# Kernel optimization log

Hardware: AMD Instinct MI355X
Metric: run time of the kernel (lower is better)

## Reference

```python
import jax, jax.numpy as jnp
import numpy as np

D_HIDN = 768
N_HEAD = 12
D_HEAD = 64
LN_EPS = 1e-5


def setup_inputs() -> dict:
    key = jax.random.key(0)
    ks = jax.random.split(key, 16)
    B, S, D = 4, 2048, D_HIDN
    s = 0.02
    inputs = jax.random.normal(ks[0], (B, S, D), dtype=jnp.float32)
    attn_mask = jax.random.uniform(ks[1], (B, S, S)) < 0.1
    Wq = jax.random.normal(ks[2], (D, D), jnp.float32) * s
    bq = jnp.zeros((D,), jnp.float32)
    Wk = jax.random.normal(ks[3], (D, D), jnp.float32) * s
    bk = jnp.zeros((D,), jnp.float32)
    Wv = jax.random.normal(ks[4], (D, D), jnp.float32) * s
    bv = jnp.zeros((D,), jnp.float32)
    g1 = jnp.ones((D,), jnp.float32)
    beta1 = jnp.zeros((D,), jnp.float32)
    W1 = jax.random.normal(ks[5], (D, 4 * D), jnp.float32) * s
    b1 = jnp.zeros((4 * D,), jnp.float32)
    W2 = jax.random.normal(ks[6], (4 * D, D), jnp.float32) * s
    b2 = jnp.zeros((D,), jnp.float32)
    g2 = jnp.ones((D,), jnp.float32)
    beta2 = jnp.zeros((D,), jnp.float32)
    return dict(inputs=inputs, attn_mask=attn_mask, Wq=Wq, bq=bq, Wk=Wk, bk=bk,
                Wv=Wv, bv=bv, g1=g1, beta1=beta1, W1=W1, b1=b1, W2=W2, b2=b2,
                g2=g2, beta2=beta2)


def _layernorm(x, g, b):
    mu = jnp.mean(x, axis=-1, keepdims=True)
    var = jnp.mean(jnp.square(x - mu), axis=-1, keepdims=True)
    return (x - mu) * jax.lax.rsqrt(var + LN_EPS) * g + b


def reference(inputs, attn_mask, Wq, bq, Wk, bk, Wv, bv, g1, beta1,
              W1, b1, W2, b2, g2, beta2):
    B, S, D = inputs.shape
    H, Dh = N_HEAD, D_HEAD
    # QKV projections -> [B, H, S, Dh]
    q = (inputs @ Wq + bq).reshape(B, S, H, Dh).transpose(0, 2, 1, 3)
    k = (inputs @ Wk + bk).reshape(B, S, H, Dh).transpose(0, 2, 1, 3)
    v = (inputs @ Wv + bv).reshape(B, S, H, Dh).transpose(0, 2, 1, 3)
    scale = 1.0 / (Dh ** 0.5)
    scores = jnp.einsum('bhqd,bhkd->bhqk', q, k) * scale  # [B,H,S,S]
    scores = jnp.where(attn_mask[:, None, :, :], jnp.float32(-1e9), scores)
    attn = jax.nn.softmax(scores, axis=-1)
    ctx = jnp.einsum('bhqk,bhkd->bhqd', attn, v)  # [B,H,S,Dh]
    attn_out = ctx.transpose(0, 2, 1, 3).reshape(B, S, D)
    # Add & Norm 1
    ffn_in = _layernorm(attn_out + inputs, g1, beta1)
    # FFN (note: no activation in the original module)
    ffn_out = (ffn_in @ W1 + b1) @ W2 + b2
    # Add & Norm 2
    return _layernorm(ffn_out + ffn_in, g2, beta2)
```

## Files before the change

kernel.cpp:

```cpp
#include <hip/hip_runtime.h>

typedef unsigned short u16;
typedef __attribute__((ext_vector_type(8))) __bf16 bf16x8;
typedef __attribute__((ext_vector_type(4))) __bf16 bf16x4;
typedef __attribute__((ext_vector_type(4))) float f32x4;

#define DEV __device__ __forceinline__

DEV u16 f2bf(float f) {
  unsigned u = __builtin_bit_cast(unsigned, f);
  u += 0x7FFFu + ((u >> 16) & 1u);
  return (u16)(u >> 16);
}
DEV float bf2f(u16 u) {
  unsigned v = (unsigned)u << 16;
  return __builtin_bit_cast(float, v);
}

DEV void stage16(const void* g, void* l) {
  __builtin_amdgcn_global_load_lds((const __attribute__((address_space(1))) void*)g,
                                   (__attribute__((address_space(3))) void*)l, 16, 0, 0);
}

DEV f32x4 mfma32(bf16x8 a, bf16x8 b, f32x4 c) {
  return __builtin_amdgcn_mfma_f32_16x16x32_bf16(a, b, c, 0, 0, 0);
}

DEV void transpose_tile(const float* __restrict__ src, u16* __restrict__ dst,
                        int R, int C, int bx, int by, int t, float (*tile)[33]) {
  int tx = t & 31, ty = t >> 5;
  int c0 = bx * 32, r0 = by * 32;
#pragma unroll
  for (int i = 0; i < 4; ++i)
    tile[ty + i * 8][tx] = src[(size_t)(r0 + ty + i * 8) * C + c0 + tx];
  __syncthreads();
#pragma unroll
  for (int i = 0; i < 4; ++i)
    dst[(size_t)(c0 + ty + i * 8) * R + r0 + tx] = f2bf(tile[tx][ty + i * 8]);
}

__global__ __launch_bounds__(256) void prep_all(
    const float* __restrict__ Wq, const float* __restrict__ Wk, const float* __restrict__ Wv,
    const float* __restrict__ W1, const float* __restrict__ W2,
    const float* __restrict__ inputs, const int* __restrict__ maskI,
    u16* __restrict__ WqkvT, u16* __restrict__ W1b, u16* __restrict__ W2T,
    u16* __restrict__ Xb, unsigned long long* __restrict__ bits) {
  __shared__ float tile[32][33];
  const int t = threadIdx.x;
  const int bid = blockIdx.x;
  if (bid < 1728) {
    int z = bid / 576, rem = bid % 576;
    const float* src = (z == 0) ? Wq : (z == 1 ? Wk : Wv);
    transpose_tile(src, WqkvT + (size_t)z * 768 * 768, 768, 768, rem % 24, rem / 24, t, tile);
  } else if (bid < 4032) {
    int rem = bid - 1728;
    transpose_tile(W2, W2T, 3072, 768, rem % 24, rem / 24, t, tile);
  } else if (bid < 6336) {
    int i = (bid - 4032) * 256 + t;
    float4 f = ((const float4*)W1)[i];
    ushort4 u;
    u.x = f2bf(f.x); u.y = f2bf(f.y); u.z = f2bf(f.z); u.w = f2bf(f.w);
    ((ushort4*)W1b)[i] = u;
  } else if (bid < 12480) {
    int i = (bid - 6336) * 256 + t;
    float4 f = ((const float4*)inputs)[i];
    ushort4 u;
    u.x = f2bf(f.x); u.y = f2bf(f.y); u.z = f2bf(f.z); u.w = f2bf(f.w);
    ((ushort4*)Xb)[i] = u;
  } else {
    int lb = bid - 12480;
    int lane = t & 63;
    int w0 = (lb * 4 + (t >> 6)) * 4;
#pragma unroll
    for (int j = 0; j < 4; ++j) {
      int v = maskI[(size_t)(w0 + j) * 64 + lane];
      unsigned long long bm = __ballot(v != 0);
      if (lane == 0) bits[w0 + j] = bm;
    }
  }
}

template <int MODE>
DEV void gemm_body(u16 (*Als)[128 * 32], u16 (*Bls)[128 * 32],
                   const u16* __restrict__ A, const u16* __restrict__ Bt, int K,
                   const float* __restrict__ b0, const float* __restrict__ b1p,
                   const float* __restrict__ b2p, const u16* __restrict__ resid,
                   u16* __restrict__ outQ, u16* __restrict__ outK, u16* __restrict__ outV,
                   u16* __restrict__ outB, int bx, int by, int bz) {
  const int t = threadIdx.x;
  const int lane = t & 63, wv = t >> 6;
  const int wm = wv & 1, wn = wv >> 1;
  const int lrow = lane & 15, g = lane >> 4;
  const int m0 = by * 128, n0 = bx * 128;

  int koff = 0, klen = K;
  if (MODE == 2) {
    klen = K >> 1;
    koff = bz * klen;
  }

  f32x4 acc[4][4] = {};

  const int idx0 = t, idx1 = 256 + t;
  const int row0 = idx0 >> 2, sl0 = (idx0 & 3) ^ ((row0 >> 1) & 3);
  const int row1 = idx1 >> 2, sl1 = (idx1 & 3) ^ ((row1 >> 1) & 3);

  auto stage = [&](int k0, int buf) {
    stage16(A + (size_t)(m0 + row0) * K + koff + k0 + sl0 * 8, (char*)Als[buf] + idx0 * 16);
    stage16(Bt + (size_t)(n0 + row0) * K + koff + k0 + sl0 * 8, (char*)Bls[buf] + idx0 * 16);
    stage16(A + (size_t)(m0 + row1) * K + koff + k0 + sl1 * 8, (char*)Als[buf] + idx1 * 16);
    stage16(Bt + (size_t)(n0 + row1) * K + koff + k0 + sl1 * 8, (char*)Bls[buf] + idx1 * 16);
  };

  stage(0, 0);
  __syncthreads();

  int nk = klen >> 5;
  for (int it = 0; it < nk; ++it) {
    int cur = it & 1;
    if (it + 1 < nk) stage((it + 1) << 5, cur ^ 1);
    bf16x8 af[4], bfr[4];
#pragma unroll
    for (int mi = 0; mi < 4; ++mi) {
      int r = wm * 64 + mi * 16 + lrow;
      int sl = g ^ ((r >> 1) & 3);
      af[mi] = *(const bf16x8*)((const char*)Als[cur] + r * 64 + sl * 16);
    }
#pragma unroll
    for (int ni = 0; ni < 4; ++ni) {
      int r = wn * 64 + ni * 16 + lrow;
      int sl = g ^ ((r >> 1) & 3);
      bfr[ni] = *(const bf16x8*)((const char*)Bls[cur] + r * 64 + sl * 16);
    }
    __builtin_amdgcn_s_setprio(1);
#pragma unroll
    for (int mi = 0; mi < 4; ++mi)
#pragma unroll
      for (int ni = 0; ni < 4; ++ni)
        acc[mi][ni] = mfma32(af[mi], bfr[ni], acc[mi][ni]);
    __builtin_amdgcn_s_setprio(0);
    __syncthreads();
  }

#pragma unroll
  for (int mi = 0; mi < 4; ++mi)
#pragma unroll
    for (int ni = 0; ni < 4; ++ni)
#pragma unroll
      for (int reg = 0; reg < 4; ++reg) {
        int gm = m0 + wm * 64 + mi * 16 + g * 4 + reg;
        int gn = n0 + wn * 64 + ni * 16 + lrow;
        float v = acc[mi][ni][reg];
        if (MODE == 0) {
          int p = gn / 768, nn = gn - p * 768;
          const float* bb = (p == 0) ? b0 : (p == 1 ? b1p : b2p);
          v += bb[nn];
          int b = gm >> 11, s = gm & 2047;
          int h = nn >> 6, dh = nn & 63;
          size_t hh = (size_t)(b * 12 + h);
          if (p == 0)      outQ[(hh * 2048 + s) * 64 + dh] = f2bf(v * 0.1803368801f);
          else if (p == 1) outK[(hh * 2048 + s) * 64 + dh] = f2bf(v);
          else             outV[(hh * 64 + dh) * 2048 + s] = f2bf(v);
        } else if (MODE == 2) {
          if (bz == 1) {
            v += b0[gn] + bf2f(resid[(size_t)gm * 768 + gn]);
            outK[(size_t)gm * 768 + gn] = f2bf(v);
          } else {
            outQ[(size_t)gm * 768 + gn] = f2bf(v);
          }
        } else {
          outB[(size_t)gn * 768 + gm] = f2bf(v);
        }
      }
}

template <int MODE, int OCC>
__global__ __launch_bounds__(256, OCC) void gemm_k(
    const u16* __restrict__ A, const u16* __restrict__ Bt, int K,
    const float* __restrict__ b0, const u16* __restrict__ resid,
    u16* __restrict__ out0, u16* __restrict__ out1) {
  __shared__ u16 Als[2][128 * 32];
  __shared__ u16 Bls[2][128 * 32];
  gemm_body<MODE>(Als, Bls, A, Bt, K, b0, nullptr, nullptr, resid,
                  out0, out1, nullptr, nullptr, blockIdx.x, blockIdx.y, blockIdx.z);
}

__global__ __launch_bounds__(256, 4) void fused_gemms(
    const u16* __restrict__ Xb, const u16* __restrict__ WqkvT,
    const float* __restrict__ bq, const float* __restrict__ bk, const float* __restrict__ bv,
    u16* __restrict__ Qb, u16* __restrict__ Kb, u16* __restrict__ Vtb,
    const u16* __restrict__ W1b, const u16* __restrict__ W2T, u16* __restrict__ W12T,
    const float* __restrict__ b1, const float* __restrict__ b2, float* __restrict__ biasEff) {
  __shared__ u16 Als[2][128 * 32];
  __shared__ u16 Bls[2][128 * 32];
  const int bid = blockIdx.x;
  if (bid < 1152) {
    gemm_body<0>(Als, Bls, Xb, WqkvT, 768, bq, bk, bv, nullptr,
                 Qb, Kb, Vtb, nullptr, bid % 18, bid / 18, 0);
  } else if (bid < 1188) {
    int lb = bid - 1152;
    gemm_body<3>(Als, Bls, W1b, W2T, 3072, nullptr, nullptr, nullptr, nullptr,
                 nullptr, nullptr, nullptr, W12T, lb % 6, lb / 6, 0);
  } else {
    const int j = bid - 1188, t = threadIdx.x;
    float s = 0.f;
    for (int k = t; k < 3072; k += 256) s += b1[k] * bf2f(W2T[(size_t)j * 3072 + k]);
    for (int d = 1; d < 64; d <<= 1) s += __shfl_xor(s, d, 64);
    __shared__ float red[4];
    if ((t & 63) == 0) red[t >> 6] = s;
    __syncthreads();
    if (t == 0) biasEff[j] = b2[j] + red[0] + red[1] + red[2] + red[3];
  }
}

__global__ __launch_bounds__(512, 6) void attn_fwd(
    const u16* __restrict__ Q, const u16* __restrict__ Kg, const u16* __restrict__ Vt,
    const unsigned long long* __restrict__ mbits, u16* __restrict__ attn_out) {
  __shared__ u16 Kls[2][64 * 64];
  __shared__ u16 Vls[2][64 * 64];
  __shared__ u16 Pls[8][16 * 64];
  const int t = threadIdx.x, lane = t & 63, wv = t >> 6;
  const int lrow = lane & 15, g = lane >> 4;

  const int fid = blockIdx.x;
  const int swz = (fid & 7) * 96 + (fid >> 3);
  const int bh = swz >> 4, q0 = (swz & 15) * 128;
  const int b = bh / 12, h = bh % 12;
  const u16* Qh = Q + (size_t)bh * 2048 * 64;
  const u16* Kh = Kg + (size_t)bh * 2048 * 64;
  const u16* Vh = Vt + (size_t)bh * 64 * 2048;

  const int qr = q0 + wv * 16 + lrow;
  bf16x8 aq[2];
  aq[0] = *(const bf16x8*)(Qh + (size_t)qr * 64 + g * 8);
  aq[1] = *(const bf16x8*)(Qh + (size_t)qr * 64 + 32 + g * 8);

  bf16x8 ones;
#pragma unroll
  for (int j = 0; j < 8; ++j) ones[j] = (__bf16)1.0f;

  f32x4 acc[4] = {};
  f32x4 lacc = {};

  const int row0 = t >> 3, sl0 = (t & 7) ^ (row0 & 7);
  auto stage = [&](int kt, int buf) {
    stage16(Kh + ((size_t)(kt * 64 + row0)) * 64 + sl0 * 8, (char*)Kls[buf] + t * 16);
    stage16(Vh + (size_t)row0 * 2048 + kt * 64 + sl0 * 8, (char*)Vls[buf] + t * 16);
  };

  const unsigned long long* mrow = mbits + ((size_t)b * 2048 + qr) * 32;
  unsigned long long mb = mrow[0];

  stage(0, 0);
  __syncthreads();

#pragma unroll 2
  for (int kt = 0; kt < 32; ++kt) {
    const int cur = kt & 1;
    if (kt + 1 < 32) stage(kt + 1, cur ^ 1);

    f32x4 sc[4];
#pragma unroll
    for (int c = 0; c < 4; ++c) {
      sc[c] = 0.f;
#pragma unroll
      for (int ks = 0; ks < 2; ++ks) {
        int r = c * 16 + lrow;
        int sl = (ks * 4 + g) ^ (r & 7);
        bf16x8 bk = *(const bf16x8*)((const char*)Kls[cur] + r * 128 + sl * 16);
        sc[c] = mfma32(bk, aq[ks], sc[c]);
      }
    }

    unsigned long long mbn = (kt + 1 < 32) ? mrow[kt + 1] : 0;

    unsigned mlo = (unsigned)mb, mhi = (unsigned)(mb >> 32);
#pragma unroll
    for (int c = 0; c < 4; ++c) {
      unsigned bits = ((c & 2) ? mhi : mlo) >> ((c & 1) * 16 + 4 * g);
#pragma unroll
      for (int reg = 0; reg < 4; ++reg)
        sc[c][reg] = ((bits >> reg) & 1) ? 0.f : __builtin_amdgcn_exp2f(sc[c][reg]);
    }
    mb = mbn;

#pragma unroll
    for (int c = 0; c < 4; ++c) {
      bf16x4 pk;
#pragma unroll
      for (int reg = 0; reg < 4; ++reg) pk[reg] = (__bf16)sc[c][reg];
      int slot = 2 * c + (g >> 1);
      int byte = lrow * 128 + ((slot ^ (lrow & 7)) << 4) + (g & 1) * 8;
      *(bf16x4*)((char*)Pls[wv] + byte) = pk;
    }
    asm volatile("s_waitcnt lgkmcnt(0)" ::: "memory");

#pragma unroll
    for (int ks = 0; ks < 2; ++ks) {
      int slp = (ks * 4 + g) ^ (lrow & 7);
      bf16x8 pa = *(const bf16x8*)((const char*)Pls[wv] + lrow * 128 + slp * 16);
      lacc = mfma32(pa, ones, lacc);
#pragma unroll
      for (int c = 0; c < 4; ++c) {
        int r = c * 16 + lrow;
        int sl = (ks * 4 + g) ^ (r & 7);
        bf16x8 vf = *(const bf16x8*)((const char*)Vls[cur] + r * 128 + sl * 16);
        acc[c] = mfma32(pa, vf, acc[c]);
      }
    }
    __syncthreads();
  }

  float rl[4];
#pragma unroll
  for (int reg = 0; reg < 4; ++reg) rl[reg] = 1.0f / lacc[reg];
#pragma unroll
  for (int c = 0; c < 4; ++c)
#pragma unroll
    for (int reg = 0; reg < 4; ++reg) {
      int q = q0 + wv * 16 + 4 * g + reg;
      int col = h * 64 + c * 16 + lrow;
      attn_out[((size_t)b * 2048 + q) * 768 + col] = f2bf(acc[c][reg] * rl[reg]);
    }
}

__global__ __launch_bounds__(192) void ln_fused2(
    const u16* __restrict__ x1b, const u16* __restrict__ x2b,
    const float* __restrict__ gam, const float* __restrict__ bet,
    float* __restrict__ outf, u16* __restrict__ outb) {
  const int row = blockIdx.x, t = threadIdx.x;
  const size_t base = (size_t)row * 768 + t * 4;
  bf16x4 a = *(const bf16x4*)(x1b + base);
  bf16x4 c = *(const bf16x4*)(x2b + base);
  float v[4], s = 0.f;
#pragma unroll
  for (int j = 0; j < 4; ++j) { v[j] = (float)a[j] + (float)c[j]; s += v[j]; }
  __shared__ float red[3];
  for (int d = 1; d < 64; d <<= 1) s += __shfl_xor(s, d, 64);
  if ((t & 63) == 0) red[t >> 6] = s;
  __syncthreads();
  s = red[0] + red[1] + red[2];
  float mu = s * (1.f / 768.f);
  float sq = 0.f;
#pragma unroll
  for (int j = 0; j < 4; ++j) { float d = v[j] - mu; sq += d * d; }
  __syncthreads();
  for (int d = 1; d < 64; d <<= 1) sq += __shfl_xor(sq, d, 64);
  if ((t & 63) == 0) red[t >> 6] = sq;
  __syncthreads();
  sq = red[0] + red[1] + red[2];
  float rs = rsqrtf(sq * (1.f / 768.f) + 1e-5f);
  const int i0 = t * 4;
  float y[4];
#pragma unroll
  for (int j = 0; j < 4; ++j) y[j] = (v[j] - mu) * rs * gam[i0 + j] + bet[i0 + j];
  if (outf) {
    float4 o = make_float4(y[0], y[1], y[2], y[3]);
    *(float4*)(outf + base) = o;
  }
  if (outb) {
    ushort4 u;
    u.x = f2bf(y[0]); u.y = f2bf(y[1]); u.z = f2bf(y[2]); u.w = f2bf(y[3]);
    *(ushort4*)(outb + base) = u;
  }
}

extern "C" void kernel_launch(void* const* d_in, const int* in_sizes, int n_in,
                              void* d_out, int out_size, void* d_ws, size_t ws_size,
                              hipStream_t stream) {
  const float* inputs = (const float*)d_in[0];
  const int*   maskI  = (const int*)d_in[1];
  const float* Wq = (const float*)d_in[2];  const float* bq = (const float*)d_in[3];
  const float* Wk = (const float*)d_in[4];  const float* bk = (const float*)d_in[5];
  const float* Wv = (const float*)d_in[6];  const float* bv = (const float*)d_in[7];
  const float* g1 = (const float*)d_in[8];  const float* be1 = (const float*)d_in[9];
  const float* W1 = (const float*)d_in[10]; const float* b1 = (const float*)d_in[11];
  const float* W2 = (const float*)d_in[12]; const float* b2 = (const float*)d_in[13];
  const float* g2 = (const float*)d_in[14]; const float* be2 = (const float*)d_in[15];
  float* out = (float*)d_out;

  char* w = (char*)d_ws;
  auto take = [&](size_t n) { char* p = w; w += (n + 255) & ~(size_t)255; return p; };
  u16* WqkvT = (u16*)take((size_t)2304 * 768 * 2);
  u16* W1b   = (u16*)take((size_t)768 * 3072 * 2);
  u16* W2T   = (u16*)take((size_t)768 * 3072 * 2);
  u16* W12T  = (u16*)take((size_t)768 * 768 * 2);
  float* biasEff = (float*)take((size_t)768 * 4);
  u16* Xb    = (u16*)take((size_t)8192 * 768 * 2);
  u16* Qb    = (u16*)take((size_t)48 * 2048 * 64 * 2);
  u16* Kb    = (u16*)take((size_t)48 * 2048 * 64 * 2);
  u16* Vtb   = (u16*)take((size_t)48 * 64 * 2048 * 2);
  unsigned long long* mbits = (unsigned long long*)take((size_t)4 * 2048 * 32 * 8);
  u16*   attnB   = (u16*)take((size_t)8192 * 768 * 2);
  u16*   ffnB    = (u16*)take((size_t)8192 * 768 * 2);
  if ((size_t)(w - (char*)d_ws) > ws_size) return;
  u16* pre0b = Qb;
  u16* pre1b = Kb;

  prep_all<<<28864, 256, 0, stream>>>(Wq, Wk, Wv, W1, W2, inputs, maskI,
                                      WqkvT, W1b, W2T, Xb, mbits);
  fused_gemms<<<1956, 256, 0, stream>>>(Xb, WqkvT, bq, bk, bv, Qb, Kb, Vtb,
                                        W1b, W2T, W12T, b1, b2, biasEff);
  attn_fwd<<<768, 512, 0, stream>>>(Qb, Kb, Vtb, mbits, attnB);
  ln_fused2<<<8192, 192, 0, stream>>>(attnB, Xb, g1, be1, nullptr, ffnB);
  gemm_k<2, 4><<<dim3(6, 64, 2), 256, 0, stream>>>(ffnB, W12T, 768, biasEff, ffnB,
                                                   pre0b, pre1b);
  ln_fused2<<<8192, 192, 0, stream>>>(pre0b, pre1b, g2, be2, out, nullptr);
}
```

Measured before the change: 271.6 us.

## Split-K the W1·W2 weight-product GEMM eightfold and schedule it first

The 36 long-K (3072) blocks that compute the fused FFN weight W1·W2 are replaced by 288 split-K blocks, each covering one eighth of K. They are placed at the start of the fused launch so they no longer form a long tail after the QKV projection blocks. The partial products are written as fp32 to a new workspace buffer. A new reduction kernel then sums the eight partials and converts the result to bf16. In exchange it adds about 19 MB of extra fp32 traffic and one more kernel launch.

```diff
diff --git a/kernel.cpp b/kernel.cpp
--- a/kernel.cpp
+++ b/kernel.cpp
@@ -86,7 +86,7 @@
                    const float* __restrict__ b0, const float* __restrict__ b1p,
                    const float* __restrict__ b2p, const u16* __restrict__ resid,
                    u16* __restrict__ outQ, u16* __restrict__ outK, u16* __restrict__ outV,
-                   u16* __restrict__ outB, int bx, int by, int bz) {
+                   float* __restrict__ outP, int bx, int by, int bz) {
   const int t = threadIdx.x;
   const int lane = t & 63, wv = t >> 6;
   const int wm = wv & 1, wn = wv >> 1;
@@ -94,10 +94,8 @@
   const int m0 = by * 128, n0 = bx * 128;
 
   int koff = 0, klen = K;
-  if (MODE == 2) {
-    klen = K >> 1;
-    koff = bz * klen;
-  }
+  if (MODE == 2) { klen = K >> 1; koff = bz * klen; }
+  if (MODE == 4) { klen = K >> 3; koff = bz * klen; }
 
   f32x4 acc[4][4] = {};
 
@@ -169,7 +167,7 @@
             outQ[(size_t)gm * 768 + gn] = f2bf(v);
           }
         } else {
-          outB[(size_t)gn * 768 + gm] = f2bf(v);
+          outP[(size_t)gn * 768 + gm] = v;
         }
       }
 }
@@ -189,20 +187,22 @@
     const u16* __restrict__ Xb, const u16* __restrict__ WqkvT,
     const float* __restrict__ bq, const float* __restrict__ bk, const float* __restrict__ bv,
     u16* __restrict__ Qb, u16* __restrict__ Kb, u16* __restrict__ Vtb,
-    const u16* __restrict__ W1b, const u16* __restrict__ W2T, u16* __restrict__ W12T,
+    const u16* __restrict__ W1b, const u16* __restrict__ W2T, float* __restrict__ W12P,
     const float* __restrict__ b1, const float* __restrict__ b2, float* __restrict__ biasEff) {
   __shared__ u16 Als[2][128 * 32];
   __shared__ u16 Bls[2][128 * 32];
   const int bid = blockIdx.x;
-  if (bid < 1152) {
+  if (bid < 288) {
+    int z = bid / 36, tl = bid % 36;
+    gemm_body<4>(Als, Bls, W1b, W2T, 3072, nullptr, nullptr, nullptr, nullptr,
+                 nullptr, nullptr, nullptr, W12P + (size_t)z * 768 * 768,
+                 tl % 6, tl / 6, z);
+  } else if (bid < 1440) {
+    int lb = bid - 288;
     gemm_body<0>(Als, Bls, Xb, WqkvT, 768, bq, bk, bv, nullptr,
-                 Qb, Kb, Vtb, nullptr, bid % 18, bid / 18, 0);
-  } else if (bid < 1188) {
-    int lb = bid - 1152;
-    gemm_body<3>(Als, Bls, W1b, W2T, 3072, nullptr, nullptr, nullptr, nullptr,
-                 nullptr, nullptr, nullptr, W12T, lb % 6, lb / 6, 0);
+                 Qb, Kb, Vtb, nullptr, lb % 18, lb / 18, 0);
   } else {
-    const int j = bid - 1188, t = threadIdx.x;
+    const int j = bid - 1440, t = threadIdx.x;
     float s = 0.f;
     for (int k = t; k < 3072; k += 256) s += b1[k] * bf2f(W2T[(size_t)j * 3072 + k]);
     for (int d = 1; d < 64; d <<= 1) s += __shfl_xor(s, d, 64);
@@ -211,6 +211,20 @@
     __syncthreads();
     if (t == 0) biasEff[j] = b2[j] + red[0] + red[1] + red[2] + red[3];
   }
+}
+
+__global__ __launch_bounds__(256) void w12_reduce(
+    const float* __restrict__ p, u16* __restrict__ W12T) {
+  const int i = blockIdx.x * 256 + threadIdx.x;
+  float4 s = ((const float4*)p)[i];
+#pragma unroll
+  for (int z = 1; z < 8; ++z) {
+    float4 q = ((const float4*)(p + (size_t)z * 768 * 768))[i];
+    s.x += q.x; s.y += q.y; s.z += q.z; s.w += q.w;
+  }
+  ushort4 u;
+  u.x = f2bf(s.x); u.y = f2bf(s.y); u.z = f2bf(s.z); u.w = f2bf(s.w);
+  ((ushort4*)W12T)[i] = u;
 }
 
 __global__ __launch_bounds__(512, 6) void attn_fwd(
@@ -385,6 +399,7 @@
   u16* W1b   = (u16*)take((size_t)768 * 3072 * 2);
   u16* W2T   = (u16*)take((size_t)768 * 3072 * 2);
   u16* W12T  = (u16*)take((size_t)768 * 768 * 2);
+  float* W12P = (float*)take((size_t)8 * 768 * 768 * 4);
   float* biasEff = (float*)take((size_t)768 * 4);
   u16* Xb    = (u16*)take((size_t)8192 * 768 * 2);
   u16* Qb    = (u16*)take((size_t)48 * 2048 * 64 * 2);
@@ -399,8 +414,9 @@
 
   prep_all<<<28864, 256, 0, stream>>>(Wq, Wk, Wv, W1, W2, inputs, maskI,
                                       WqkvT, W1b, W2T, Xb, mbits);
-  fused_gemms<<<1956, 256, 0, stream>>>(Xb, WqkvT, bq, bk, bv, Qb, Kb, Vtb,
-                                        W1b, W2T, W12T, b1, b2, biasEff);
+  fused_gemms<<<2208, 256, 0, stream>>>(Xb, WqkvT, bq, bk, bv, Qb, Kb, Vtb,
+                                        W1b, W2T, W12P, b1, b2, biasEff);
+  w12_reduce<<<576, 256, 0, stream>>>(W12P, W12T);
   attn_fwd<<<768, 512, 0, stream>>>(Qb, Kb, Vtb, mbits, attnB);
   ln_fused2<<<8192, 192, 0, stream>>>(attnB, Xb, g1, be1, nullptr, ffnB);
   gemm_k<2, 4><<<dim3(6, 64, 2), 256, 0, stream>>>(ffnB, W12T, 768, biasEff, ffnB,
```

Measured after the change: 245.2 us. 1.11x faster.
